# Performance work log

Hardware: AMD Instinct MI355X
Metric: run time of the kernel (lower is better)

The kernel has to match this reference:

```python
import jax, jax.numpy as jnp
import numpy as np

B, D_IN, H, T_EMB = 16384, 256, 512, 16


def _lin_params(key, out_dim, in_dim, bias):
    k1, k2 = jax.random.split(key)
    s = 1.0 / np.sqrt(in_dim)
    W = jax.random.uniform(k1, (out_dim, in_dim), jnp.float32, -s, s)
    b = jax.random.uniform(k2, (out_dim,), jnp.float32, -s, s) if bias else None
    return W, b


def setup_inputs() -> dict:
    key = jax.random.key(0)
    ks = jax.random.split(key, 20)
    x = jax.random.normal(ks[0], (B, D_IN), jnp.float32)
    h = jax.random.normal(ks[1], (B, H), jnp.float32)
    c_prev = jax.random.normal(ks[2], (B, H), jnp.float32)
    delt = jax.random.uniform(ks[3], (B, T_EMB), jnp.float32)

    W_ix, b_ix = _lin_params(ks[4], H, D_IN, True)
    W_ih, _ = _lin_params(ks[5], H, H, False)
    W_ic, _ = _lin_params(ks[6], H, H, False)
    W_fx, b_fx = _lin_params(ks[7], H, D_IN, True)
    W_fh, _ = _lin_params(ks[8], H, H, False)
    W_fc, _ = _lin_params(ks[9], H, H, False)
    W_tx, b_tx = _lin_params(ks[10], H, D_IN, True)
    W_tt, _ = _lin_params(ks[11], H, T_EMB, False)
    W_cx, b_cx = _lin_params(ks[12], H, D_IN, True)
    W_ch, _ = _lin_params(ks[13], H, H, False)
    W_ox, b_ox = _lin_params(ks[14], H, D_IN, True)
    W_oh, _ = _lin_params(ks[15], H, H, False)
    W_oc, _ = _lin_params(ks[16], H, H, False)
    W_ot, _ = _lin_params(ks[17], H, T_EMB, False)

    return dict(x=x, h=h, c_prev=c_prev, delt=delt,
                W_ix=W_ix, b_ix=b_ix, W_ih=W_ih, W_ic=W_ic,
                W_fx=W_fx, b_fx=b_fx, W_fh=W_fh, W_fc=W_fc,
                W_tx=W_tx, b_tx=b_tx, W_tt=W_tt,
                W_cx=W_cx, b_cx=b_cx, W_ch=W_ch,
                W_ox=W_ox, b_ox=b_ox, W_oh=W_oh, W_oc=W_oc, W_ot=W_ot)


def reference(x, h, c_prev, delt,
              W_ix, b_ix, W_ih, W_ic,
              W_fx, b_fx, W_fh, W_fc,
              W_tx, b_tx, W_tt,
              W_cx, b_cx, W_ch,
              W_ox, b_ox, W_oh, W_oc, W_ot):
    sig, tanh = jax.nn.sigmoid, jnp.tanh
    # input gate
    i = sig(x @ W_ix.T + b_ix + h @ W_ih.T + c_prev @ W_ic.T)
    # forget gate
    f = sig(x @ W_fx.T + b_fx + h @ W_fh.T + c_prev @ W_fc.T)
    # time gate: note inner sigmoid on the time-delta projection
    T = sig(x @ W_tx.T + b_tx + sig(delt @ W_tt.T))
    # candidate cell and new cell state
    k = tanh(x @ W_cx.T + b_cx + h @ W_ch.T)
    c_next = i * T * k + f * c_prev
    # output gate
    o = sig(x @ W_ox.T + b_ox + delt @ W_ot.T + h @ W_oh.T + c_prev @ W_oc.T)
    h_next = o * tanh(c_next)
    return (h_next, c_next, T)
```

## Files before the change

kernel.cpp:

```cpp
#include <hip/hip_runtime.h>
#include <cstdint>

#define B_SZ   16384
#define H_SZ   512
#define DIN    256
#define TEMB   16
#define KP     1344
#define KPB    1344
#define BH     8388608L
#define SLOT   26624
#define GSTR   688128

typedef __attribute__((ext_vector_type(4))) float f32x4;
typedef __attribute__((ext_vector_type(4))) int   i32x4;

typedef const __attribute__((address_space(1))) unsigned int gu32_t;
typedef __attribute__((address_space(3)))       unsigned int lu32_t;

__device__ constexpr int RG[6] = {0, 1, 4, 3, 2, 4};

__device__ __forceinline__ void gld16(const void* g, void* l) {
  __builtin_amdgcn_global_load_lds((gu32_t*)(uintptr_t)g,
                                   (lu32_t*)(unsigned int)(uintptr_t)l, 16, 0, 0);
}

__device__ __forceinline__ float sigm(float v)  { return 1.0f / (1.0f + __expf(-v)); }
__device__ __forceinline__ float tanhx(float v) { return 2.0f / (1.0f + __expf(-2.0f * v)) - 1.0f; }

__device__ __forceinline__ signed char q8(float v, float inv) {
  int q = __float2int_rn(v * inv);
  q = (q > 127) ? 127 : (q < -127 ? -127 : q);
  return (signed char)q;
}

__global__ void prep_a8_kernel(const float* __restrict__ x, const float* __restrict__ h,
                               const float* __restrict__ c, const float* __restrict__ dl,
                               signed char* __restrict__ Ap, float* __restrict__ sa) {
  __shared__ float row[KP];
  __shared__ float red[256];
  const int m   = blockIdx.x;
  const int tid = threadIdx.x;
  float lmax = 0.f;
  for (int i = tid; i < KP / 4; i += 256) {
    const int k4 = i * 4;
    float4 v = make_float4(0.f, 0.f, 0.f, 0.f);
    if (k4 < 256)       v = *(const float4*)(x  + (size_t)m * DIN  + k4);
    else if (k4 < 768)  v = *(const float4*)(h  + (size_t)m * H_SZ + (k4 - 256));
    else if (k4 < 1280) v = *(const float4*)(c  + (size_t)m * H_SZ + (k4 - 768));
    else if (k4 < 1296) v = *(const float4*)(dl + (size_t)m * TEMB + (k4 - 1280));
    *(float4*)(row + k4) = v;
    lmax = fmaxf(lmax, fmaxf(fmaxf(fabsf(v.x), fabsf(v.y)), fmaxf(fabsf(v.z), fabsf(v.w))));
  }
  red[tid] = lmax;
  __syncthreads();
  for (int s = 128; s > 0; s >>= 1) {
    if (tid < s) red[tid] = fmaxf(red[tid], red[tid + s]);
    __syncthreads();
  }
  const float smax = fmaxf(red[0], 1e-20f);
  const float inv  = 127.0f / smax;
  if (tid == 0) sa[m] = smax * (1.0f / 127.0f);
  for (int i = tid; i < KP / 4; i += 256) {
    const int k4 = i * 4;
    char4 o;
    o.x = q8(row[k4],     inv); o.y = q8(row[k4 + 1], inv);
    o.z = q8(row[k4 + 2], inv); o.w = q8(row[k4 + 3], inv);
    *(char4*)(Ap + (size_t)m * KPB + k4) = o;
  }
}

__global__ void prep_w8_kernel(const float* __restrict__ Wix, const float* __restrict__ Wih, const float* __restrict__ Wic,
                               const float* __restrict__ Wfx, const float* __restrict__ Wfh, const float* __restrict__ Wfc,
                               const float* __restrict__ Wtx, const float* __restrict__ Wtt,
                               const float* __restrict__ Wcx, const float* __restrict__ Wch,
                               const float* __restrict__ Wox, const float* __restrict__ Woh,
                               const float* __restrict__ Woc, const float* __restrict__ Wot,
                               signed char* __restrict__ Wp, float* __restrict__ sw) {
  __shared__ float row[KP];
  __shared__ float red[256];
  const int R   = blockIdx.x;
  const int g   = R >> 9;
  const int n   = R & 511;
  const int tid = threadIdx.x;
  float lmax = 0.f;
  for (int i = tid; i < KP / 4; i += 256) {
    const int k4 = i * 4;
    const float* src = nullptr; long o = 0;
    if (g == 0) {
      if (k4 < 256)       { src = Wix; o = (long)n * 256 + k4; }
      else if (k4 < 768)  { src = Wih; o = (long)n * 512 + (k4 - 256); }
      else if (k4 < 1280) { src = Wic; o = (long)n * 512 + (k4 - 768); }
    } else if (g == 1) {
      if (k4 < 256)       { src = Wfx; o = (long)n * 256 + k4; }
      else if (k4 < 768)  { src = Wfh; o = (long)n * 512 + (k4 - 256); }
      else if (k4 < 1280) { src = Wfc; o = (long)n * 512 + (k4 - 768); }
    } else if (g == 2) {
      if (k4 < 256)       { src = Wtx; o = (long)n * 256 + k4; }
    } else if (g == 3) {
      if (k4 < 256)       { src = Wcx; o = (long)n * 256 + k4; }
      else if (k4 < 768)  { src = Wch; o = (long)n * 512 + (k4 - 256); }
    } else if (g == 4) {
      if (k4 < 256)       { src = Wox; o = (long)n * 256 + k4; }
      else if (k4 < 768)  { src = Woh; o = (long)n * 512 + (k4 - 256); }
      else if (k4 < 1280) { src = Woc; o = (long)n * 512 + (k4 - 768); }
      else if (k4 < 1296) { src = Wot; o = (long)n * 16 + (k4 - 1280); }
    } else {
      if (k4 >= 1280 && k4 < 1296) { src = Wtt; o = (long)n * 16 + (k4 - 1280); }
    }
    float4 v = make_float4(0.f, 0.f, 0.f, 0.f);
    if (src) v = *(const float4*)(src + o);
    *(float4*)(row + k4) = v;
    lmax = fmaxf(lmax, fmaxf(fmaxf(fabsf(v.x), fabsf(v.y)), fmaxf(fabsf(v.z), fabsf(v.w))));
  }
  red[tid] = lmax;
  __syncthreads();
  for (int s = 128; s > 0; s >>= 1) {
    if (tid < s) red[tid] = fmaxf(red[tid], red[tid + s]);
    __syncthreads();
  }
  const float smax = fmaxf(red[0], 1e-20f);
  const float inv  = 127.0f / smax;
  if (tid == 0) sw[R] = smax * (1.0f / 127.0f);
  for (int i = tid; i < KP / 4; i += 256) {
    const int k4 = i * 4;
    char4 o;
    o.x = q8(row[k4],     inv); o.y = q8(row[k4 + 1], inv);
    o.z = q8(row[k4 + 2], inv); o.w = q8(row[k4 + 3], inv);
    *(char4*)(Wp + (size_t)R * KPB + k4) = o;
  }
}


template<unsigned SMASK>
__device__ __forceinline__ void stage(char* lds, int sb, int ht,
                                      const char* sAb, const char* sWb, int wid) {
  const unsigned kb = (unsigned)ht * 64u;
  gld16(sAb + kb,              lds + sb + wid * 2048);
  gld16(sAb + kb + 16u * KPB,  lds + sb + wid * 2048 + 1024);
#pragma unroll
  for (int g = 0; g < 6; ++g) {
    if (SMASK & (1u << g)) {
#pragma unroll
      for (int c = 0; c < 2; ++c) {
        if (((2 * g + c) & 7) == wid)
          gld16(sWb + (unsigned)g * GSTR + (unsigned)c * (16u * KPB) + kb,
                lds + sb + 16384 + RG[g] * 2048 + c * 1024);
      }
    }
  }
}

template<unsigned CM>
__device__ __forceinline__ void comp(const char* lds, int sb, int aro, int wro,
                                     i32x4 acc[6][4]) {
  const char* base = lds + sb;
  i32x4 a[4];
#pragma unroll
  for (int i = 0; i < 4; ++i)
    a[i] = *(const i32x4*)(base + aro + i * 1024);
  __builtin_amdgcn_s_setprio(1);
#pragma unroll
  for (int g = 0; g < 6; ++g) {
    if (CM & (1u << g)) {
      i32x4 b = *(const i32x4*)(base + 16384 + RG[g] * 2048 + wro);
#pragma unroll
      for (int i = 0; i < 4; ++i)
        acc[g][i] = __builtin_amdgcn_mfma_i32_16x16x64_i8(a[i], b, acc[g][i], 0, 0, 0);
    }
  }
  __builtin_amdgcn_s_setprio(0);
}

template<unsigned CM, unsigned SM, bool ST>
__device__ __forceinline__ void phase(char* lds, int h, const char* sAb, const char* sWb,
                                      int wid, int aro, int wro, i32x4 acc[6][4]) {
  if (ST) stage<SM>(lds, ((h + 1) & 1) * SLOT, h + 1, sAb, sWb, wid);
  comp<CM>(lds, (h & 1) * SLOT, aro, wro, acc);
  __syncthreads();
}

__global__ __launch_bounds__(512, 4) void lstm_main(
    const signed char* __restrict__ Ap, const signed char* __restrict__ Wp,
    const float* __restrict__ sa, const float* __restrict__ sw,
    const float* __restrict__ c_prev,
    const float* __restrict__ b_ix, const float* __restrict__ b_fx,
    const float* __restrict__ b_tx, const float* __restrict__ b_cx,
    const float* __restrict__ b_ox,
    float* __restrict__ out)
{
  __shared__ __align__(16) char lds[2 * SLOT];

  const int tid  = threadIdx.x;
  const int lane = tid & 63;
  const int wid  = tid >> 6;

  const int bid = blockIdx.x;
  const int xcd = bid & 7;
  const int idx = bid >> 3;
  const int cb  = (xcd << 1) | (idx & 1);
  const int rb  = idx >> 1;
  const unsigned brow = (unsigned)rb * 256u;
  const int bcol = cb * 32;

  const int wr  = (wid >> 1) * 64;
  const int wcg = (wid & 1) * 16;
  const int lrow = lane & 15;
  const int kgrp = lane >> 4;

  i32x4 acc[6][4];
  {
    i32x4 z = {0, 0, 0, 0};
#pragma unroll
    for (int g = 0; g < 6; ++g)
#pragma unroll
      for (int i = 0; i < 4; ++i) acc[g][i] = z;
  }

  const int sread = ((kgrp + (lrow >> 1)) & 3) << 4;
  const int aro = (wr + lrow) * 64 + sread;
  const int wro = (wcg + lrow) * 64 + sread;

  const int l4 = lane >> 2;
  const int kslot = (((lane & 3) - ((lane >> 3) & 3)) & 3) << 4;
  const char* sAb = (const char*)Ap + (size_t)(brow + wid * 32 + l4) * KPB + kslot;
  const char* sWb = (const char*)Wp + (size_t)(bcol + l4) * KPB + kslot;

  stage<0x1F>(lds, 0, 0, sAb, sWb, wid);
  __syncthreads();

#pragma unroll 1
  for (int h = 0; h < 3; ++h)
    phase<0x1F, 0x1F, true>(lds, h, sAb, sWb, wid, aro, wro, acc);
  phase<0x1F, 0x1B, true>(lds, 3, sAb, sWb, wid, aro, wro, acc);
#pragma unroll 1
  for (int h = 4; h < 11; ++h)
    phase<0x1B, 0x1B, true>(lds, h, sAb, sWb, wid, aro, wro, acc);
  phase<0x1B, 0x13, true>(lds, 11, sAb, sWb, wid, aro, wro, acc);
#pragma unroll 1
  for (int h = 12; h < 19; ++h)
    phase<0x13, 0x13, true>(lds, h, sAb, sWb, wid, aro, wro, acc);
  phase<0x13, 0x30, true>(lds, 19, sAb, sWb, wid, aro, wro, acc);
  comp<0x30>(lds, (20 & 1) * SLOT, aro, wro, acc);

  const int n = bcol + wcg + lrow;
  const float bi  = b_ix[n], bff = b_fx[n], bt = b_tx[n], bc = b_cx[n], bo = b_ox[n];
  const float s0 = sw[0 * 512 + n], s1 = sw[1 * 512 + n], s2 = sw[2 * 512 + n];
  const float s3 = sw[3 * 512 + n], s4 = sw[4 * 512 + n], s5 = sw[5 * 512 + n];
  const int rbase = kgrp * 4;
#pragma unroll
  for (int i = 0; i < 4; ++i) {
    const int m0 = (int)brow + wr + 16 * i + rbase;
    const float4 sa4 = *(const float4*)(sa + m0);
#pragma unroll
    for (int r = 0; r < 4; ++r) {
      const long m   = m0 + r;
      const long off = m * H_SZ + n;
      const float sr = (r == 0) ? sa4.x : (r == 1) ? sa4.y : (r == 2) ? sa4.z : sa4.w;
      const float iv = sigm((float)acc[0][i][r] * sr * s0 + bi);
      const float fv = sigm((float)acc[1][i][r] * sr * s1 + bff);
      const float Tv = sigm((float)acc[2][i][r] * sr * s2 + bt
                            + sigm((float)acc[5][i][r] * sr * s5));
      const float kv = tanhx((float)acc[3][i][r] * sr * s3 + bc);
      const float ov = sigm((float)acc[4][i][r] * sr * s4 + bo);
      const float cp = c_prev[off];
      const float cn = iv * Tv * kv + fv * cp;
      out[off]          = ov * tanhx(cn);
      out[BH + off]     = cn;
      out[2 * BH + off] = Tv;
    }
  }
}

extern "C" void kernel_launch(void* const* d_in, const int* in_sizes, int n_in,
                              void* d_out, int out_size, void* d_ws, size_t ws_size,
                              hipStream_t stream) {
  const float* x      = (const float*)d_in[0];
  const float* h      = (const float*)d_in[1];
  const float* c_prev = (const float*)d_in[2];
  const float* dl     = (const float*)d_in[3];
  const float* W_ix = (const float*)d_in[4];
  const float* b_ix = (const float*)d_in[5];
  const float* W_ih = (const float*)d_in[6];
  const float* W_ic = (const float*)d_in[7];
  const float* W_fx = (const float*)d_in[8];
  const float* b_fx = (const float*)d_in[9];
  const float* W_fh = (const float*)d_in[10];
  const float* W_fc = (const float*)d_in[11];
  const float* W_tx = (const float*)d_in[12];
  const float* b_tx = (const float*)d_in[13];
  const float* W_tt = (const float*)d_in[14];
  const float* W_cx = (const float*)d_in[15];
  const float* b_cx = (const float*)d_in[16];
  const float* W_ch = (const float*)d_in[17];
  const float* W_ox = (const float*)d_in[18];
  const float* b_ox = (const float*)d_in[19];
  const float* W_oh = (const float*)d_in[20];
  const float* W_oc = (const float*)d_in[21];
  const float* W_ot = (const float*)d_in[22];

  signed char* Ap8 = (signed char*)d_ws;
  signed char* Wp8 = (signed char*)d_ws + (size_t)B_SZ * KPB;
  float* sa = (float*)((char*)d_ws + (size_t)B_SZ * KPB + 6L * H_SZ * KPB);
  float* sw = sa + B_SZ;

  prep_a8_kernel<<<B_SZ, 256, 0, stream>>>(x, h, c_prev, dl, Ap8, sa);
  prep_w8_kernel<<<6 * H_SZ, 256, 0, stream>>>(
      W_ix, W_ih, W_ic, W_fx, W_fh, W_fc, W_tx, W_tt, W_cx, W_ch,
      W_ox, W_oh, W_oc, W_ot, Wp8, sw);

  lstm_main<<<1024, 512, 0, stream>>>(Ap8, Wp8, sa, sw, c_prev,
                                      b_ix, b_fx, b_tx, b_cx, b_ox,
                                      (float*)d_out);
}
```

Baseline: 123.2 us.

## Split time-gate GEMM into separate short kernel, shrink main kernel to four gates

The time gate only depends on x and delt, i.e. the first four K-tiles plus the delta tile. It is moved into its own kernel that stages only those tiles for the two time-gate weight blocks and writes T directly into the output buffer. The main kernel then keeps four gate accumulators instead of six, uses a smaller LDS slot and a simpler staging map, and reads T back from global memory. This frees registers and LDS and removes the unbalanced staging, at the cost of an extra launch and an extra round trip of T through memory.

```diff
diff --git a/kernel.cpp b/kernel.cpp
--- a/kernel.cpp
+++ b/kernel.cpp
@@ -8,7 +8,8 @@
 #define KP     1344
 #define KPB    1344
 #define BH     8388608L
-#define SLOT   26624
+#define SLOT   24576
+#define TSLOT  20480
 #define GSTR   688128
 
 typedef __attribute__((ext_vector_type(4))) float f32x4;
@@ -16,8 +17,6 @@
 
 typedef const __attribute__((address_space(1))) unsigned int gu32_t;
 typedef __attribute__((address_space(3)))       unsigned int lu32_t;
-
-__device__ constexpr int RG[6] = {0, 1, 4, 3, 2, 4};
 
 __device__ __forceinline__ void gld16(const void* g, void* l) {
   __builtin_amdgcn_global_load_lds((gu32_t*)(uintptr_t)g,
@@ -137,22 +136,17 @@
   const unsigned kb = (unsigned)ht * 64u;
   gld16(sAb + kb,              lds + sb + wid * 2048);
   gld16(sAb + kb + 16u * KPB,  lds + sb + wid * 2048 + 1024);
-#pragma unroll
-  for (int g = 0; g < 6; ++g) {
-    if (SMASK & (1u << g)) {
-#pragma unroll
-      for (int c = 0; c < 2; ++c) {
-        if (((2 * g + c) & 7) == wid)
-          gld16(sWb + (unsigned)g * GSTR + (unsigned)c * (16u * KPB) + kb,
-                lds + sb + 16384 + RG[g] * 2048 + c * 1024);
-      }
-    }
+  const int r = wid >> 1, c = wid & 1;
+  if (SMASK & (1u << r)) {
+    const int g = r + (r >> 1);
+    gld16(sWb + (unsigned)g * GSTR + (unsigned)c * (16u * KPB) + kb,
+          lds + sb + 16384 + r * 2048 + c * 1024);
   }
 }
 
 template<unsigned CM>
 __device__ __forceinline__ void comp(const char* lds, int sb, int aro, int wro,
-                                     i32x4 acc[6][4]) {
+                                     i32x4 acc[4][4]) {
   const char* base = lds + sb;
   i32x4 a[4];
 #pragma unroll
@@ -160,12 +154,12 @@
     a[i] = *(const i32x4*)(base + aro + i * 1024);
   __builtin_amdgcn_s_setprio(1);
 #pragma unroll
-  for (int g = 0; g < 6; ++g) {
-    if (CM & (1u << g)) {
-      i32x4 b = *(const i32x4*)(base + 16384 + RG[g] * 2048 + wro);
+  for (int r = 0; r < 4; ++r) {
+    if (CM & (1u << r)) {
+      i32x4 b = *(const i32x4*)(base + 16384 + r * 2048 + wro);
 #pragma unroll
       for (int i = 0; i < 4; ++i)
-        acc[g][i] = __builtin_amdgcn_mfma_i32_16x16x64_i8(a[i], b, acc[g][i], 0, 0, 0);
+        acc[r][i] = __builtin_amdgcn_mfma_i32_16x16x64_i8(a[i], b, acc[r][i], 0, 0, 0);
     }
   }
   __builtin_amdgcn_s_setprio(0);
@@ -173,7 +167,7 @@
 
 template<unsigned CM, unsigned SM, bool ST>
 __device__ __forceinline__ void phase(char* lds, int h, const char* sAb, const char* sWb,
-                                      int wid, int aro, int wro, i32x4 acc[6][4]) {
+                                      int wid, int aro, int wro, i32x4 acc[4][4]) {
   if (ST) stage<SM>(lds, ((h + 1) & 1) * SLOT, h + 1, sAb, sWb, wid);
   comp<CM>(lds, (h & 1) * SLOT, aro, wro, acc);
   __syncthreads();
@@ -184,8 +178,7 @@
     const float* __restrict__ sa, const float* __restrict__ sw,
     const float* __restrict__ c_prev,
     const float* __restrict__ b_ix, const float* __restrict__ b_fx,
-    const float* __restrict__ b_tx, const float* __restrict__ b_cx,
-    const float* __restrict__ b_ox,
+    const float* __restrict__ b_cx, const float* __restrict__ b_ox,
     float* __restrict__ out)
 {
   __shared__ __align__(16) char lds[2 * SLOT];
@@ -207,11 +200,11 @@
   const int lrow = lane & 15;
   const int kgrp = lane >> 4;
 
-  i32x4 acc[6][4];
+  i32x4 acc[4][4];
   {
     i32x4 z = {0, 0, 0, 0};
 #pragma unroll
-    for (int g = 0; g < 6; ++g)
+    for (int g = 0; g < 4; ++g)
 #pragma unroll
       for (int i = 0; i < 4; ++i) acc[g][i] = z;
   }
@@ -225,27 +218,24 @@
   const char* sAb = (const char*)Ap + (size_t)(brow + wid * 32 + l4) * KPB + kslot;
   const char* sWb = (const char*)Wp + (size_t)(bcol + l4) * KPB + kslot;
 
-  stage<0x1F>(lds, 0, 0, sAb, sWb, wid);
+  stage<0xF>(lds, 0, 0, sAb, sWb, wid);
   __syncthreads();
 
 #pragma unroll 1
-  for (int h = 0; h < 3; ++h)
-    phase<0x1F, 0x1F, true>(lds, h, sAb, sWb, wid, aro, wro, acc);
-  phase<0x1F, 0x1B, true>(lds, 3, sAb, sWb, wid, aro, wro, acc);
-#pragma unroll 1
-  for (int h = 4; h < 11; ++h)
-    phase<0x1B, 0x1B, true>(lds, h, sAb, sWb, wid, aro, wro, acc);
-  phase<0x1B, 0x13, true>(lds, 11, sAb, sWb, wid, aro, wro, acc);
+  for (int h = 0; h < 11; ++h)
+    phase<0xF, 0xF, true>(lds, h, sAb, sWb, wid, aro, wro, acc);
+  phase<0xF, 0xB, true>(lds, 11, sAb, sWb, wid, aro, wro, acc);
 #pragma unroll 1
   for (int h = 12; h < 19; ++h)
-    phase<0x13, 0x13, true>(lds, h, sAb, sWb, wid, aro, wro, acc);
-  phase<0x13, 0x30, true>(lds, 19, sAb, sWb, wid, aro, wro, acc);
-  comp<0x30>(lds, (20 & 1) * SLOT, aro, wro, acc);
-
+    phase<0xB, 0xB, true>(lds, h, sAb, sWb, wid, aro, wro, acc);
+  phase<0xB, 0x8, true>(lds, 19, sAb, sWb, wid, aro, wro, acc);
+  comp<0x8>(lds, (20 & 1) * SLOT, aro, wro, acc);
+
+  const float* Tvp = out + 2 * BH;
   const int n = bcol + wcg + lrow;
-  const float bi  = b_ix[n], bff = b_fx[n], bt = b_tx[n], bc = b_cx[n], bo = b_ox[n];
-  const float s0 = sw[0 * 512 + n], s1 = sw[1 * 512 + n], s2 = sw[2 * 512 + n];
-  const float s3 = sw[3 * 512 + n], s4 = sw[4 * 512 + n], s5 = sw[5 * 512 + n];
+  const float bi = b_ix[n], bff = b_fx[n], bc = b_cx[n], bo = b_ox[n];
+  const float s0 = sw[0 * 512 + n], s1 = sw[1 * 512 + n];
+  const float s3 = sw[3 * 512 + n], s4 = sw[4 * 512 + n];
   const int rbase = kgrp * 4;
 #pragma unroll
   for (int i = 0; i < 4; ++i) {
@@ -258,15 +248,124 @@
       const float sr = (r == 0) ? sa4.x : (r == 1) ? sa4.y : (r == 2) ? sa4.z : sa4.w;
       const float iv = sigm((float)acc[0][i][r] * sr * s0 + bi);
       const float fv = sigm((float)acc[1][i][r] * sr * s1 + bff);
-      const float Tv = sigm((float)acc[2][i][r] * sr * s2 + bt
-                            + sigm((float)acc[5][i][r] * sr * s5));
-      const float kv = tanhx((float)acc[3][i][r] * sr * s3 + bc);
-      const float ov = sigm((float)acc[4][i][r] * sr * s4 + bo);
+      const float kv = tanhx((float)acc[2][i][r] * sr * s3 + bc);
+      const float ov = sigm((float)acc[3][i][r] * sr * s4 + bo);
+      const float Tv = Tvp[off];
       const float cp = c_prev[off];
       const float cn = iv * Tv * kv + fv * cp;
-      out[off]          = ov * tanhx(cn);
-      out[BH + off]     = cn;
-      out[2 * BH + off] = Tv;
+      out[off]      = ov * tanhx(cn);
+      out[BH + off] = cn;
+    }
+  }
+}
+
+template<unsigned SMASK>
+__device__ __forceinline__ void stage_t(char* lds, int sb, int ht,
+                                        const char* sAb, const char* sWb, int wid) {
+  const unsigned kb = (unsigned)ht * 64u;
+  gld16(sAb + kb,              lds + sb + wid * 2048);
+  gld16(sAb + kb + 16u * KPB,  lds + sb + wid * 2048 + 1024);
+  if (wid < 4) {
+    const int r = wid >> 1, c = wid & 1;
+    if (SMASK & (1u << r)) {
+      const int g = (r == 0) ? 2 : 5;
+      gld16(sWb + (unsigned)g * GSTR + (unsigned)c * (16u * KPB) + kb,
+            lds + sb + 16384 + r * 2048 + c * 1024);
+    }
+  }
+}
+
+template<unsigned CM>
+__device__ __forceinline__ void comp_t(const char* lds, int sb, int aro, int wro,
+                                       i32x4 acc[2][4]) {
+  const char* base = lds + sb;
+  i32x4 a[4];
+#pragma unroll
+  for (int i = 0; i < 4; ++i)
+    a[i] = *(const i32x4*)(base + aro + i * 1024);
+#pragma unroll
+  for (int r = 0; r < 2; ++r) {
+    if (CM & (1u << r)) {
+      i32x4 b = *(const i32x4*)(base + 16384 + r * 2048 + wro);
+#pragma unroll
+      for (int i = 0; i < 4; ++i)
+        acc[r][i] = __builtin_amdgcn_mfma_i32_16x16x64_i8(a[i], b, acc[r][i], 0, 0, 0);
+    }
+  }
+}
+
+__global__ __launch_bounds__(512, 4) void tgate_kernel(
+    const signed char* __restrict__ Ap, const signed char* __restrict__ Wp,
+    const float* __restrict__ sa, const float* __restrict__ sw,
+    const float* __restrict__ b_tx, float* __restrict__ out)
+{
+  __shared__ __align__(16) char lds[2 * TSLOT];
+
+  const int tid  = threadIdx.x;
+  const int lane = tid & 63;
+  const int wid  = tid >> 6;
+
+  const int bid = blockIdx.x;
+  const int xcd = bid & 7;
+  const int idx = bid >> 3;
+  const int cb  = (xcd << 1) | (idx & 1);
+  const int rb  = idx >> 1;
+  const unsigned brow = (unsigned)rb * 256u;
+  const int bcol = cb * 32;
+
+  const int wr  = (wid >> 1) * 64;
+  const int wcg = (wid & 1) * 16;
+  const int lrow = lane & 15;
+  const int kgrp = lane >> 4;
+
+  i32x4 acc[2][4];
+  {
+    i32x4 z = {0, 0, 0, 0};
+#pragma unroll
+    for (int g = 0; g < 2; ++g)
+#pragma unroll
+      for (int i = 0; i < 4; ++i) acc[g][i] = z;
+  }
+
+  const int sread = ((kgrp + (lrow >> 1)) & 3) << 4;
+  const int aro = (wr + lrow) * 64 + sread;
+  const int wro = (wcg + lrow) * 64 + sread;
+
+  const int l4 = lane >> 2;
+  const int kslot = (((lane & 3) - ((lane >> 3) & 3)) & 3) << 4;
+  const char* sAb = (const char*)Ap + (size_t)(brow + wid * 32 + l4) * KPB + kslot;
+  const char* sWb = (const char*)Wp + (size_t)(bcol + l4) * KPB + kslot;
+
+  stage_t<0x1>(lds, 0, 0, sAb, sWb, wid);
+  __syncthreads();
+  stage_t<0x1>(lds, TSLOT, 1, sAb, sWb, wid);
+  comp_t<0x1>(lds, 0, aro, wro, acc);
+  __syncthreads();
+  stage_t<0x1>(lds, 0, 2, sAb, sWb, wid);
+  comp_t<0x1>(lds, TSLOT, aro, wro, acc);
+  __syncthreads();
+  stage_t<0x1>(lds, TSLOT, 3, sAb, sWb, wid);
+  comp_t<0x1>(lds, 0, aro, wro, acc);
+  __syncthreads();
+  stage_t<0x2>(lds, 0, 20, sAb, sWb, wid);
+  comp_t<0x1>(lds, TSLOT, aro, wro, acc);
+  __syncthreads();
+  comp_t<0x2>(lds, 0, aro, wro, acc);
+
+  const int n = bcol + wcg + lrow;
+  const float bt = b_tx[n];
+  const float s2 = sw[2 * 512 + n], s5 = sw[5 * 512 + n];
+  const int rbase = kgrp * 4;
+#pragma unroll
+  for (int i = 0; i < 4; ++i) {
+    const int m0 = (int)brow + wr + 16 * i + rbase;
+    const float4 sa4 = *(const float4*)(sa + m0);
+#pragma unroll
+    for (int r = 0; r < 4; ++r) {
+      const long off = (long)(m0 + r) * H_SZ + n;
+      const float sr = (r == 0) ? sa4.x : (r == 1) ? sa4.y : (r == 2) ? sa4.z : sa4.w;
+      const float inner = sigm((float)acc[1][i][r] * sr * s5);
+      out[2 * BH + off] = sigm((float)acc[0][i][r] * sr * s2 + bt + inner);
     }
   }
 }
@@ -308,7 +407,9 @@
       W_ix, W_ih, W_ic, W_fx, W_fh, W_fc, W_tx, W_tt, W_cx, W_ch,
       W_ox, W_oh, W_oc, W_ot, Wp8, sw);
 
+  tgate_kernel<<<1024, 512, 0, stream>>>(Ap8, Wp8, sa, sw, b_tx, (float*)d_out);
+
   lstm_main<<<1024, 512, 0, stream>>>(Ap8, Wp8, sa, sw, c_prev,
-                                      b_ix, b_fx, b_tx, b_cx, b_ox,
+                                      b_ix, b_fx, b_cx, b_ox,
                                       (float*)d_out);
 }
```

Measured after the change: 130.3 us. 5.7% more time.

## Merge activation and weight quantization into one launch with wave-per-row prep

Applied to the files above, without the earlier changes.

The two int8 prep kernels become a single launch. The first 4096 blocks quantize activations with one 64-lane wave per row, keeping values in registers and reducing the row max with shuffles instead of shared memory and barriers. The remaining blocks do weight quantization as before. This removes one kernel launch and the LDS round-trip and syncs in activation prep, at the cost of more registers per thread and a branchy combined kernel.

```diff
diff --git a/kernel.cpp b/kernel.cpp
--- a/kernel.cpp
+++ b/kernel.cpp
@@ -33,55 +33,56 @@
   return (signed char)q;
 }
 
-__global__ void prep_a8_kernel(const float* __restrict__ x, const float* __restrict__ h,
-                               const float* __restrict__ c, const float* __restrict__ dl,
-                               signed char* __restrict__ Ap, float* __restrict__ sa) {
+__global__ void prep_kernel(const float* __restrict__ x, const float* __restrict__ h,
+                            const float* __restrict__ c, const float* __restrict__ dl,
+                            const float* __restrict__ Wix, const float* __restrict__ Wih, const float* __restrict__ Wic,
+                            const float* __restrict__ Wfx, const float* __restrict__ Wfh, const float* __restrict__ Wfc,
+                            const float* __restrict__ Wtx, const float* __restrict__ Wtt,
+                            const float* __restrict__ Wcx, const float* __restrict__ Wch,
+                            const float* __restrict__ Wox, const float* __restrict__ Woh,
+                            const float* __restrict__ Woc, const float* __restrict__ Wot,
+                            signed char* __restrict__ Ap, float* __restrict__ sa,
+                            signed char* __restrict__ Wp, float* __restrict__ sw) {
   __shared__ float row[KP];
   __shared__ float red[256];
-  const int m   = blockIdx.x;
   const int tid = threadIdx.x;
-  float lmax = 0.f;
-  for (int i = tid; i < KP / 4; i += 256) {
-    const int k4 = i * 4;
-    float4 v = make_float4(0.f, 0.f, 0.f, 0.f);
-    if (k4 < 256)       v = *(const float4*)(x  + (size_t)m * DIN  + k4);
-    else if (k4 < 768)  v = *(const float4*)(h  + (size_t)m * H_SZ + (k4 - 256));
-    else if (k4 < 1280) v = *(const float4*)(c  + (size_t)m * H_SZ + (k4 - 768));
-    else if (k4 < 1296) v = *(const float4*)(dl + (size_t)m * TEMB + (k4 - 1280));
-    *(float4*)(row + k4) = v;
-    lmax = fmaxf(lmax, fmaxf(fmaxf(fabsf(v.x), fabsf(v.y)), fmaxf(fabsf(v.z), fabsf(v.w))));
-  }
-  red[tid] = lmax;
-  __syncthreads();
-  for (int s = 128; s > 0; s >>= 1) {
-    if (tid < s) red[tid] = fmaxf(red[tid], red[tid + s]);
-    __syncthreads();
-  }
-  const float smax = fmaxf(red[0], 1e-20f);
-  const float inv  = 127.0f / smax;
-  if (tid == 0) sa[m] = smax * (1.0f / 127.0f);
-  for (int i = tid; i < KP / 4; i += 256) {
-    const int k4 = i * 4;
-    char4 o;
-    o.x = q8(row[k4],     inv); o.y = q8(row[k4 + 1], inv);
-    o.z = q8(row[k4 + 2], inv); o.w = q8(row[k4 + 3], inv);
-    *(char4*)(Ap + (size_t)m * KPB + k4) = o;
-  }
-}
-
-__global__ void prep_w8_kernel(const float* __restrict__ Wix, const float* __restrict__ Wih, const float* __restrict__ Wic,
-                               const float* __restrict__ Wfx, const float* __restrict__ Wfh, const float* __restrict__ Wfc,
-                               const float* __restrict__ Wtx, const float* __restrict__ Wtt,
-                               const float* __restrict__ Wcx, const float* __restrict__ Wch,
-                               const float* __restrict__ Wox, const float* __restrict__ Woh,
-                               const float* __restrict__ Woc, const float* __restrict__ Wot,
-                               signed char* __restrict__ Wp, float* __restrict__ sw) {
-  __shared__ float row[KP];
-  __shared__ float red[256];
-  const int R   = blockIdx.x;
-  const int g   = R >> 9;
-  const int n   = R & 511;
-  const int tid = threadIdx.x;
+  if (blockIdx.x < 4096) {
+    const int lane = tid & 63;
+    const int m    = blockIdx.x * 4 + (tid >> 6);
+    float4 v[6];
+    float lmax = 0.f;
+#pragma unroll
+    for (int i = 0; i < 6; ++i) {
+      const int k4 = (i * 64 + lane) * 4;
+      float4 t = make_float4(0.f, 0.f, 0.f, 0.f);
+      if (k4 < 256)       t = *(const float4*)(x  + (size_t)m * DIN  + k4);
+      else if (k4 < 768)  t = *(const float4*)(h  + (size_t)m * H_SZ + (k4 - 256));
+      else if (k4 < 1280) t = *(const float4*)(c  + (size_t)m * H_SZ + (k4 - 768));
+      else if (k4 < 1296) t = *(const float4*)(dl + (size_t)m * TEMB + (k4 - 1280));
+      v[i] = t;
+      lmax = fmaxf(lmax, fmaxf(fmaxf(fabsf(t.x), fabsf(t.y)), fmaxf(fabsf(t.z), fabsf(t.w))));
+    }
+#pragma unroll
+    for (int s = 1; s < 64; s <<= 1)
+      lmax = fmaxf(lmax, __shfl_xor(lmax, s));
+    const float smax = fmaxf(lmax, 1e-20f);
+    const float inv  = 127.0f / smax;
+    if (lane == 0) sa[m] = smax * (1.0f / 127.0f);
+#pragma unroll
+    for (int i = 0; i < 6; ++i) {
+      const int k4 = (i * 64 + lane) * 4;
+      if (k4 < KP) {
+        char4 o;
+        o.x = q8(v[i].x, inv); o.y = q8(v[i].y, inv);
+        o.z = q8(v[i].z, inv); o.w = q8(v[i].w, inv);
+        *(char4*)(Ap + (size_t)m * KPB + k4) = o;
+      }
+    }
+    return;
+  }
+  const int R = blockIdx.x - 4096;
+  const int g = R >> 9;
+  const int n = R & 511;
   float lmax = 0.f;
   for (int i = tid; i < KP / 4; i += 256) {
     const int k4 = i * 4;
@@ -303,10 +304,10 @@
   float* sa = (float*)((char*)d_ws + (size_t)B_SZ * KPB + 6L * H_SZ * KPB);
   float* sw = sa + B_SZ;
 
-  prep_a8_kernel<<<B_SZ, 256, 0, stream>>>(x, h, c_prev, dl, Ap8, sa);
-  prep_w8_kernel<<<6 * H_SZ, 256, 0, stream>>>(
+  prep_kernel<<<4096 + 3072, 256, 0, stream>>>(
+      x, h, c_prev, dl,
       W_ix, W_ih, W_ic, W_fx, W_fh, W_fc, W_tx, W_tt, W_cx, W_ch,
-      W_ox, W_oh, W_oc, W_ot, Wp8, sw);
+      W_ox, W_oh, W_oc, W_ot, Ap8, sa, Wp8, sw);
 
   lstm_main<<<1024, 512, 0, stream>>>(Ap8, Wp8, sa, sw, c_prev,
                                       b_ix, b_fx, b_tx, b_cx, b_ox,
```

After: 110.8 us. 1.11x faster.
